# Performance work log

Measured on AMD Instinct MI355X. Metric: run time of the kernel, lower is better.

## Reference

```python
import jax, jax.numpy as jnp
import numpy as np

B, IN_DIM, HID, E, G, EPS = 8192, 1024, 2048, 16, 256, 1e-5

def setup_inputs() -> dict:
    key = jax.random.key(0)
    ks = jax.random.split(key, 8)
    s = 0.02
    f32 = jnp.float32
    return {
        "x": jax.random.normal(ks[0], (B, IN_DIM), f32),
        "g_ln_w": jnp.ones((IN_DIM,), f32),
        "g_ln_b": jnp.zeros((IN_DIM,), f32),
        "g_w1": jax.random.normal(ks[1], (IN_DIM, G), f32) * s,
        "g_b1": jnp.zeros((G,), f32),
        "g_w2": jax.random.normal(ks[2], (G, E), f32) * s,
        "g_b2": jnp.zeros((E,), f32),
        "e_ln_w": jnp.ones((E, IN_DIM), f32),
        "e_ln_b": jnp.zeros((E, IN_DIM), f32),
        "e_w1": jax.random.normal(ks[3], (E, IN_DIM, HID), f32) * s,
        "e_b1": jnp.zeros((E, HID), f32),
        "e_w2": jax.random.normal(ks[4], (E, HID, G), f32) * s,
        "e_b2": jnp.zeros((E, G), f32),
        "e_w3": jax.random.normal(ks[5], (E, G, 2), f32) * s,
        "e_b3": jnp.zeros((E, 2), f32),
    }

def reference(x, g_ln_w, g_ln_b, g_w1, g_b1, g_w2, g_b2,
              e_ln_w, e_ln_b, e_w1, e_b1, e_w2, e_b2, e_w3, e_b3):
    # Shared normalization (all LayerNorms normalize the same x), per-module affine.
    mu = jnp.mean(x, axis=-1, keepdims=True)
    var = jnp.mean((x - mu) ** 2, axis=-1, keepdims=True)
    xhat = (x - mu) * jax.lax.rsqrt(var + EPS)            # [B, D]
    # Gate: LN -> Linear(256) -> ReLU -> Linear(E) -> softmax
    gh = jax.nn.relu((xhat * g_ln_w + g_ln_b) @ g_w1 + g_b1)
    gate_w = jax.nn.softmax(gh @ g_w2 + g_b2, axis=-1)    # [B, E]
    # All experts batched over leading E axis (dropout = identity in eval)
    xe = xhat[None] * e_ln_w[:, None, :] + e_ln_b[:, None, :]              # [E, B, D]
    h1 = jax.nn.relu(jnp.einsum('ebd,edh->ebh', xe, e_w1) + e_b1[:, None, :])  # [E, B, HID]
    h2 = jax.nn.relu(jnp.einsum('ebh,ehg->ebg', h1, e_w2) + e_b2[:, None, :])  # [E, B, G]
    oe = jnp.einsum('ebg,ego->ebo', h2, e_w3) + e_b3[:, None, :]               # [E, B, 2]
    out = jnp.einsum('ebo,be->bo', oe, gate_w)                                  # [B, 2]
    pred_mean = out[:, 0:1]
    pred_var = jax.nn.softplus(out[:, 1:2]) + 1e-6
    return (pred_mean, pred_var)
```

## Files before the change

kernel.cpp:

```cpp
#include <hip/hip_runtime.h>

#define B_ 8192
#define D_ 1024
#define H_ 2048
#define E_ 16
#define G_ 256

typedef unsigned short u16;
typedef __attribute__((ext_vector_type(4))) float f32x4;
typedef __attribute__((ext_vector_type(8))) short bf16x8;
typedef __attribute__((ext_vector_type(4))) unsigned short u16x4;

__device__ u16   g_W1t[(size_t)E_ * H_ * D_];
__device__ u16   g_W2t[(size_t)E_ * G_ * H_];
__device__ u16   g_GW1t[(size_t)G_ * D_];
__device__ u16   g_xhat[(size_t)B_ * D_];
__device__ u16   g_gh[(size_t)B_ * G_];
__device__ float g_b1part[4 * E_ * H_];
__device__ float g_b1p[E_ * H_];
__device__ float g_gb1part[4 * G_];
__device__ float g_gb1p[G_];
__device__ float g_gate[(size_t)B_ * E_];
__device__ float g_oep[(size_t)E_ * B_ * 2];

__device__ __forceinline__ u16 f2bf(float f) {
  unsigned int u = __float_as_uint(f);
  unsigned int r = (u + 0x7fffu + ((u >> 16) & 1u)) >> 16;
  return (u16)r;
}
__device__ __forceinline__ float bf2f(u16 u) {
  return __uint_as_float((unsigned int)u << 16);
}
__device__ __forceinline__ void gld16(const void* g, void* l) {
  __builtin_amdgcn_global_load_lds(
      (const __attribute__((address_space(1))) unsigned int*)g,
      (__attribute__((address_space(3))) unsigned int*)l, 16, 0, 0);
}

__global__ __launch_bounds__(256) void k_transpose_scale(
    const float* __restrict__ src, const float* __restrict__ scale,
    int which, int R, int C) {
  u16* dstb = (which == 0) ? g_W1t : (which == 1) ? g_W2t : g_GW1t;
  __shared__ float tile[32][33];
  int z = blockIdx.z;
  const float* s = src + (size_t)z * R * C;
  u16* d = dstb + (size_t)z * R * C;
  int c0 = blockIdx.x * 32, r0 = blockIdx.y * 32;
#pragma unroll
  for (int i = 0; i < 4; i++) {
    int r = r0 + threadIdx.y + i * 8;
    int c = c0 + threadIdx.x;
    float v = s[(size_t)r * C + c];
    if (scale) v *= scale[(size_t)z * R + r];
    tile[threadIdx.y + i * 8][threadIdx.x] = v;
  }
  __syncthreads();
#pragma unroll
  for (int i = 0; i < 4; i++) {
    int c = c0 + threadIdx.y + i * 8;
    int r = r0 + threadIdx.x;
    d[(size_t)c * R + r] = f2bf(tile[threadIdx.x][threadIdx.y + i * 8]);
  }
}

__global__ __launch_bounds__(256) void k_prep_bias(
    const float* __restrict__ W, const float* __restrict__ lnb,
    const float* __restrict__ bias, int which, int D, int N, int Z) {
  float* part = (which == 0) ? g_b1part : g_gb1part;
  int z = blockIdx.x;
  int n = blockIdx.y * 256 + threadIdx.x;
  int dc = blockIdx.z;
  int dlen = D / 4, d0 = dc * dlen;
  const float* Wb = W + (size_t)z * D * N;
  const float* lb = lnb + (size_t)z * D;
  float acc = (dc == 0) ? bias[(size_t)z * N + n] : 0.f;
  for (int d = d0; d < d0 + dlen; d++) acc += lb[d] * Wb[(size_t)d * N + n];
  part[((size_t)dc * Z + z) * N + n] = acc;
}

__global__ __launch_bounds__(256) void k_combine_bias(int which, int len) {
  const float* part = (which == 0) ? g_b1part : g_gb1part;
  float* out = (which == 0) ? g_b1p : g_gb1p;
  int i = blockIdx.x * 256 + threadIdx.x;
  if (i < len)
    out[i] = part[i] + part[len + i] + part[2 * len + i] + part[3 * len + i];
}

__global__ __launch_bounds__(256) void k_layernorm(const float* __restrict__ x) {
  int row = blockIdx.x;
  int tid = threadIdx.x;
  const float4 v = ((const float4*)(x + (size_t)row * D_))[tid];
  float s1 = v.x + v.y + v.z + v.w;
  float s2 = v.x * v.x + v.y * v.y + v.z * v.z + v.w * v.w;
#pragma unroll
  for (int m = 1; m < 64; m <<= 1) {
    s1 += __shfl_xor(s1, m, 64);
    s2 += __shfl_xor(s2, m, 64);
  }
  __shared__ float red[8];
  int w = tid >> 6, l = tid & 63;
  if (l == 0) { red[w * 2] = s1; red[w * 2 + 1] = s2; }
  __syncthreads();
  s1 = red[0] + red[2] + red[4] + red[6];
  s2 = red[1] + red[3] + red[5] + red[7];
  float mu = s1 * (1.f / D_);
  float var = s2 * (1.f / D_) - mu * mu;
  float rs = rsqrtf(var + 1e-5f);
  u16x4 p;
  p.x = f2bf((v.x - mu) * rs);
  p.y = f2bf((v.y - mu) * rs);
  p.z = f2bf((v.z - mu) * rs);
  p.w = f2bf((v.w - mu) * rs);
  ((u16x4*)(g_xhat + (size_t)row * D_))[tid] = p;
}

__global__ __launch_bounds__(256) void k_gating_gemm() {
  __shared__ alignas(16) char pool[8192 + 16384];
  u16* A_st = (u16*)pool;
  u16* B_st = (u16*)(pool + 8192);
  const int r0 = blockIdx.x * 64;
  const int n0 = blockIdx.y * 128;
  const int tid = threadIdx.x, l = tid & 63, w = tid >> 6;
  const int l15 = l & 15, l4 = l >> 4, lx = l15 & 7;
  const int srow = tid >> 3;
  const int sk8s = (tid & 7) ^ ((tid >> 3) & 7);

  f32x4 zero4 = {0.f, 0.f, 0.f, 0.f};
  f32x4 acc[4][2];
#pragma unroll
  for (int i = 0; i < 4; i++)
#pragma unroll
    for (int j = 0; j < 2; j++) acc[i][j] = zero4;

  for (int s = 0; s < 16; s++) {
    __syncthreads();
#pragma unroll
    for (int r = 0; r < 2; r++) {
      int row = r * 32 + srow;
      gld16(g_xhat + (size_t)(r0 + row) * D_ + s * 64 + sk8s * 8,
            (char*)A_st + (r * 256 + (tid & 192)) * 16);
    }
#pragma unroll
    for (int r = 0; r < 4; r++) {
      int row = r * 32 + srow;
      gld16(g_GW1t + (size_t)(n0 + row) * D_ + s * 64 + sk8s * 8,
            (char*)B_st + (r * 256 + (tid & 192)) * 16);
    }
    __syncthreads();
#pragma unroll
    for (int t = 0; t < 2; t++) {
      bf16x8 af[4], bfr[2];
#pragma unroll
      for (int mi = 0; mi < 4; mi++)
        af[mi] = *(const bf16x8*)&A_st[(mi * 16 + l15) * 64 + ((t * 4 + l4) ^ lx) * 8];
#pragma unroll
      for (int ni = 0; ni < 2; ni++)
        bfr[ni] = *(const bf16x8*)&B_st[(w * 32 + ni * 16 + l15) * 64 + ((t * 4 + l4) ^ lx) * 8];
#pragma unroll
      for (int mi = 0; mi < 4; mi++)
#pragma unroll
        for (int ni = 0; ni < 2; ni++)
          acc[mi][ni] = __builtin_amdgcn_mfma_f32_16x16x32_bf16(
              af[mi], bfr[ni], acc[mi][ni], 0, 0, 0);
    }
  }
#pragma unroll
  for (int ni = 0; ni < 2; ni++) {
    int n = n0 + w * 32 + ni * 16 + l15;
    float bv = g_gb1p[n];
#pragma unroll
    for (int mi = 0; mi < 4; mi++)
#pragma unroll
      for (int q = 0; q < 4; q++) {
        int row = r0 + mi * 16 + l4 * 4 + q;
        g_gh[(size_t)row * G_ + n] = f2bf(fmaxf(acc[mi][ni][q] + bv, 0.f));
      }
  }
}

__global__ __launch_bounds__(256) void k_gating_softmax(
    const float* __restrict__ gw2, const float* __restrict__ gb2) {
  int tid = threadIdx.x;
  int rl = tid >> 4, j = tid & 15;
  int row = blockIdx.x * 16 + rl;
  const u16* gr = g_gh + (size_t)row * G_;
  float acc = gb2[j];
  for (int k = 0; k < G_; k++) acc += bf2f(gr[k]) * gw2[k * 16 + j];
  float m = acc;
#pragma unroll
  for (int mm = 1; mm < 16; mm <<= 1) m = fmaxf(m, __shfl_xor(m, mm, 64));
  float e = expf(acc - m);
  float s = e;
#pragma unroll
  for (int mm = 1; mm < 16; mm <<= 1) s += __shfl_xor(s, mm, 64);
  g_gate[(size_t)row * 16 + j] = e / s;
}

__global__ __launch_bounds__(256, 2) void k_chain(
    const float* __restrict__ eb2,
    const float* __restrict__ w3,
    const float* __restrict__ b3)
{
  constexpr int BM = 128, NT = 128, BK = 64;
  constexpr int C1LD = NT + 8;
  __shared__ alignas(16) char pool[32768 + BM * C1LD * 2 + 2 * BM * 2 * 4];
  u16* A_st = (u16*)pool;
  u16* B_st = (u16*)(pool + 16384);
  u16* C1 = (u16*)(pool + 32768);
  float* oeac = (float*)(pool + 32768 + BM * C1LD * 2);

  const int wg = blockIdx.x;
  const int xcd = wg & 7;
  const int idx = wg >> 3;
  const int e = idx >> 3;
  const int r0 = (xcd * 8 + (idx & 7)) * BM;

  const int tid = threadIdx.x;
  const int l = tid & 63, w = tid >> 6;
  const int wr = w >> 1, wc = w & 1;
  const int l15 = l & 15, l4 = l >> 4, lx = l15 & 7;
  const int srow = tid >> 3;
  const int sk8s = (tid & 7) ^ ((tid >> 3) & 7);

  const u16* W1e = g_W1t + (size_t)e * H_ * D_;
  const u16* W2e = g_W2t + (size_t)e * G_ * H_;

  f32x4 zero4 = {0.f, 0.f, 0.f, 0.f};
  f32x4 acc2[4][8];
#pragma unroll
  for (int i = 0; i < 4; i++)
#pragma unroll
    for (int j = 0; j < 8; j++) acc2[i][j] = zero4;

  for (int kk = 0; kk < H_ / NT; kk++) {
    f32x4 acc1[4][4];
#pragma unroll
    for (int i = 0; i < 4; i++)
#pragma unroll
      for (int j = 0; j < 4; j++) acc1[i][j] = zero4;

    for (int s = 0; s < D_ / BK; s++) {
      __syncthreads();
#pragma unroll
      for (int r = 0; r < 4; r++) {
        int row = r * 32 + srow;
        gld16(g_xhat + (size_t)(r0 + row) * D_ + s * BK + sk8s * 8,
              (char*)A_st + (r * 256 + (tid & 192)) * 16);
      }
#pragma unroll
      for (int r = 0; r < 4; r++) {
        int row = r * 32 + srow;
        gld16(W1e + (size_t)(kk * NT + row) * D_ + s * BK + sk8s * 8,
              (char*)B_st + (r * 256 + (tid & 192)) * 16);
      }
      __syncthreads();
#pragma unroll
      for (int t = 0; t < 2; t++) {
        bf16x8 af[4], bfr[4];
#pragma unroll
        for (int mi = 0; mi < 4; mi++)
          af[mi] = *(const bf16x8*)&A_st[(wr * 64 + mi * 16 + l15) * BK + ((t * 4 + l4) ^ lx) * 8];
#pragma unroll
        for (int ni = 0; ni < 4; ni++)
          bfr[ni] = *(const bf16x8*)&B_st[(wc * 64 + ni * 16 + l15) * BK + ((t * 4 + l4) ^ lx) * 8];
#pragma unroll
        for (int mi = 0; mi < 4; mi++)
#pragma unroll
          for (int ni = 0; ni < 4; ni++)
            acc1[mi][ni] = __builtin_amdgcn_mfma_f32_16x16x32_bf16(
                af[mi], bfr[ni], acc1[mi][ni], 0, 0, 0);
      }
    }
    float bn[4];
#pragma unroll
    for (int ni = 0; ni < 4; ni++)
      bn[ni] = g_b1p[e * H_ + kk * NT + wc * 64 + ni * 16 + l15];
#pragma unroll
    for (int mi = 0; mi < 4; mi++)
#pragma unroll
      for (int ni = 0; ni < 4; ni++)
#pragma unroll
        for (int q = 0; q < 4; q++) {
          float v = fmaxf(acc1[mi][ni][q] + bn[ni], 0.f);
          C1[(wr * 64 + mi * 16 + l4 * 4 + q) * C1LD + wc * 64 + ni * 16 + l15] = f2bf(v);
        }
    __syncthreads();

#pragma unroll
    for (int k2 = 0; k2 < 2; k2++) {
#pragma unroll
      for (int r = 0; r < 8; r++) {
        int grow = r * 32 + srow;
        gld16(W2e + (size_t)grow * H_ + kk * NT + k2 * 64 + sk8s * 8,
              pool + (r * 256 + (tid & 192)) * 16);
      }
      __syncthreads();
      const u16* B2 = (const u16*)pool;
#pragma unroll
      for (int t = 0; t < 2; t++) {
        bf16x8 a2[4];
#pragma unroll
        for (int mi = 0; mi < 4; mi++)
          a2[mi] = *(const bf16x8*)&C1[(wr * 64 + mi * 16 + l15) * C1LD + k2 * 64 + t * 32 + l4 * 8];
#pragma unroll
        for (int nj = 0; nj < 8; nj++) {
          bf16x8 b2 = *(const bf16x8*)&B2[(wc * 128 + nj * 16 + l15) * 64 + ((t * 4 + l4) ^ lx) * 8];
#pragma unroll
          for (int mi = 0; mi < 4; mi++)
            acc2[mi][nj] = __builtin_amdgcn_mfma_f32_16x16x32_bf16(
                a2[mi], b2, acc2[mi][nj], 0, 0, 0);
        }
      }
      __syncthreads();
    }
  }

  float w30[8], w31[8], bb[8];
#pragma unroll
  for (int nj = 0; nj < 8; nj++) {
    int g = wc * 128 + nj * 16 + l15;
    w30[nj] = w3[(e * G_ + g) * 2 + 0];
    w31[nj] = w3[(e * G_ + g) * 2 + 1];
    bb[nj] = eb2[e * G_ + g];
  }
#pragma unroll
  for (int mi = 0; mi < 4; mi++)
#pragma unroll
    for (int q = 0; q < 4; q++) {
      float s0 = 0.f, s1 = 0.f;
#pragma unroll
      for (int nj = 0; nj < 8; nj++) {
        float h = fmaxf(acc2[mi][nj][q] + bb[nj], 0.f);
        s0 += h * w30[nj];
        s1 += h * w31[nj];
      }
#pragma unroll
      for (int mm = 1; mm < 16; mm <<= 1) {
        s0 += __shfl_xor(s0, mm, 64);
        s1 += __shfl_xor(s1, mm, 64);
      }
      if (l15 == 0) {
        int row = wr * 64 + mi * 16 + l4 * 4 + q;
        oeac[(wc * BM + row) * 2 + 0] = s0;
        oeac[(wc * BM + row) * 2 + 1] = s1;
      }
    }
  __syncthreads();
  if (tid < BM) {
    int row = tid;
    float gg = g_gate[(size_t)(r0 + row) * E_ + e];
    float o0 = oeac[row * 2 + 0] + oeac[(BM + row) * 2 + 0] + b3[e * 2 + 0];
    float o1 = oeac[row * 2 + 1] + oeac[(BM + row) * 2 + 1] + b3[e * 2 + 1];
    g_oep[((size_t)e * B_ + (r0 + row)) * 2 + 0] = gg * o0;
    g_oep[((size_t)e * B_ + (r0 + row)) * 2 + 1] = gg * o1;
  }
}

__global__ __launch_bounds__(256) void k_finalize(float* __restrict__ out) {
  int i = blockIdx.x * 256 + threadIdx.x;
  float m = 0.f, v = 0.f;
#pragma unroll
  for (int e = 0; e < E_; e++) {
    m += g_oep[((size_t)e * B_ + i) * 2 + 0];
    v += g_oep[((size_t)e * B_ + i) * 2 + 1];
  }
  float sp = (v > 20.f) ? v : log1pf(expf(v));
  out[i] = m;
  out[B_ + i] = sp + 1e-6f;
}

extern "C" void kernel_launch(void* const* d_in, const int* in_sizes, int n_in,
                              void* d_out, int out_size, void* d_ws, size_t ws_size,
                              hipStream_t stream) {
  const float* x    = (const float*)d_in[0];
  const float* glnw = (const float*)d_in[1];
  const float* glnb = (const float*)d_in[2];
  const float* gw1  = (const float*)d_in[3];
  const float* gb1  = (const float*)d_in[4];
  const float* gw2  = (const float*)d_in[5];
  const float* gb2  = (const float*)d_in[6];
  const float* elnw = (const float*)d_in[7];
  const float* elnb = (const float*)d_in[8];
  const float* ew1  = (const float*)d_in[9];
  const float* eb1  = (const float*)d_in[10];
  const float* ew2  = (const float*)d_in[11];
  const float* eb2  = (const float*)d_in[12];
  const float* ew3  = (const float*)d_in[13];
  const float* eb3  = (const float*)d_in[14];
  float* out = (float*)d_out;
  (void)d_ws; (void)ws_size;

  dim3 tb(32, 8);
  k_transpose_scale<<<dim3(H_ / 32, D_ / 32, E_), tb, 0, stream>>>(ew1, elnw, 0, D_, H_);
  k_transpose_scale<<<dim3(G_ / 32, H_ / 32, E_), tb, 0, stream>>>(ew2, nullptr, 1, H_, G_);
  k_transpose_scale<<<dim3(G_ / 32, D_ / 32, 1), tb, 0, stream>>>(gw1, glnw, 2, D_, G_);

  k_prep_bias<<<dim3(E_, H_ / 256, 4), 256, 0, stream>>>(ew1, elnb, eb1, 0, D_, H_, E_);
  k_prep_bias<<<dim3(1, 1, 4), 256, 0, stream>>>(gw1, glnb, gb1, 1, D_, G_, 1);
  k_combine_bias<<<(E_ * H_ + 255) / 256, 256, 0, stream>>>(0, E_ * H_);
  k_combine_bias<<<1, 256, 0, stream>>>(1, G_);

  k_layernorm<<<B_, 256, 0, stream>>>(x);
  k_gating_gemm<<<dim3(B_ / 64, G_ / 128), 256, 0, stream>>>();
  k_gating_softmax<<<B_ / 16, 256, 0, stream>>>(gw2, gb2);

  k_chain<<<dim3(B_ / 128 * E_), 256, 0, stream>>>(eb2, ew3, eb3);

  k_finalize<<<B_ / 256, 256, 0, stream>>>(out);
}
```

Baseline: 1.341 ms.

## Double-buffer GEMM1 K-loop with async global-to-LDS prefetch and MFMA priority

```diff
diff --git a/kernel.cpp b/kernel.cpp
--- a/kernel.cpp
+++ b/kernel.cpp
@@ -201,11 +201,9 @@
     const float* __restrict__ w3,
     const float* __restrict__ b3)
 {
-  constexpr int BM = 128, NT = 128, BK = 64;
+  constexpr int BM = 128, NT = 128;
   constexpr int C1LD = NT + 8;
   __shared__ alignas(16) char pool[32768 + BM * C1LD * 2 + 2 * BM * 2 * 4];
-  u16* A_st = (u16*)pool;
-  u16* B_st = (u16*)(pool + 16384);
   u16* C1 = (u16*)(pool + 32768);
   float* oeac = (float*)(pool + 32768 + BM * C1LD * 2);
 
@@ -219,6 +217,13 @@
   const int l = tid & 63, w = tid >> 6;
   const int wr = w >> 1, wc = w & 1;
   const int l15 = l & 15, l4 = l >> 4, lx = l15 & 7;
+
+  const int srow8 = tid >> 3;
+  const int sp = (tid & 7) ^ (srow8 & 7);
+  const int shalf = sp >> 2;
+  const int sc8 = (sp & 3) * 8;
+  const int sdst = (tid & 192) * 16;
+
   const int srow = tid >> 3;
   const int sk8s = (tid & 7) ^ ((tid >> 3) & 7);
 
@@ -239,38 +244,52 @@
 #pragma unroll
       for (int j = 0; j < 4; j++) acc1[i][j] = zero4;
 
-    for (int s = 0; s < D_ / BK; s++) {
-      __syncthreads();
-#pragma unroll
-      for (int r = 0; r < 4; r++) {
-        int row = r * 32 + srow;
-        gld16(g_xhat + (size_t)(r0 + row) * D_ + s * BK + sk8s * 8,
-              (char*)A_st + (r * 256 + (tid & 192)) * 16);
-      }
-#pragma unroll
-      for (int r = 0; r < 4; r++) {
-        int row = r * 32 + srow;
-        gld16(W1e + (size_t)(kk * NT + row) * D_ + s * BK + sk8s * 8,
-              (char*)B_st + (r * 256 + (tid & 192)) * 16);
-      }
-      __syncthreads();
-#pragma unroll
-      for (int t = 0; t < 2; t++) {
-        bf16x8 af[4], bfr[4];
-#pragma unroll
-        for (int mi = 0; mi < 4; mi++)
-          af[mi] = *(const bf16x8*)&A_st[(wr * 64 + mi * 16 + l15) * BK + ((t * 4 + l4) ^ lx) * 8];
+    auto STAGE = [&](int s, int buf) {
+#pragma unroll
+      for (int i = 0; i < 4; i++) {
+        int row = srow8 + 32 * i;
+        const u16* src = shalf
+            ? (W1e + (size_t)(kk * NT + row) * D_ + s * 32 + sc8)
+            : (g_xhat + (size_t)(r0 + row) * D_ + s * 32 + sc8);
+        gld16(src, pool + buf * 16384 + i * 4096 + sdst);
+      }
+    };
+    auto CONSUME = [&](int buf) {
+      const u16* S = (const u16*)(pool + buf * 16384);
+      bf16x8 af[4], bfr[4];
+#pragma unroll
+      for (int mi = 0; mi < 4; mi++) {
+        int row = wr * 64 + mi * 16 + l15;
+        af[mi] = *(const bf16x8*)&S[row * 64 + (l4 ^ lx) * 8];
+      }
+#pragma unroll
+      for (int ni = 0; ni < 4; ni++) {
+        int row = wc * 64 + ni * 16 + l15;
+        bfr[ni] = *(const bf16x8*)&S[row * 64 + ((4 + l4) ^ lx) * 8];
+      }
+      __builtin_amdgcn_s_setprio(1);
+#pragma unroll
+      for (int mi = 0; mi < 4; mi++)
 #pragma unroll
         for (int ni = 0; ni < 4; ni++)
-          bfr[ni] = *(const bf16x8*)&B_st[(wc * 64 + ni * 16 + l15) * BK + ((t * 4 + l4) ^ lx) * 8];
-#pragma unroll
-        for (int mi = 0; mi < 4; mi++)
-#pragma unroll
-          for (int ni = 0; ni < 4; ni++)
-            acc1[mi][ni] = __builtin_amdgcn_mfma_f32_16x16x32_bf16(
-                af[mi], bfr[ni], acc1[mi][ni], 0, 0, 0);
-      }
-    }
+          acc1[mi][ni] = __builtin_amdgcn_mfma_f32_16x16x32_bf16(
+              af[mi], bfr[ni], acc1[mi][ni], 0, 0, 0);
+      __builtin_amdgcn_s_setprio(0);
+    };
+
+    STAGE(0, 0);
+    for (int s = 0; s < 31; s++) {
+      STAGE(s + 1, (s + 1) & 1);
+      asm volatile("s_waitcnt vmcnt(4)" ::: "memory");
+      asm volatile("s_barrier" ::: "memory");
+      CONSUME(s & 1);
+      asm volatile("s_barrier" ::: "memory");
+    }
+    asm volatile("s_waitcnt vmcnt(0)" ::: "memory");
+    asm volatile("s_barrier" ::: "memory");
+    CONSUME(1);
+    asm volatile("s_barrier" ::: "memory");
+
     float bn[4];
 #pragma unroll
     for (int ni = 0; ni < 4; ni++)
```

Result: slower. 1.717 ms (+28.0%).
